# Kernel tuning notes

Hardware: AMD Instinct MI355X
Metric: run time of the kernel (lower is better)

Reference implementation:

```python
import jax, jax.numpy as jnp
import numpy as np

B, L, D = 16, 1024, 1024
OUT_LEN = 24
N_LAYERS = 3
CYCLE = L
LN_EPS = 1e-5


def _make_pe(seq_len, hidden, cycle):
    # pe[t, j] = 2*pi*t/cycle, then sin on even cols, cos on odd cols
    t = jnp.arange(seq_len, dtype=jnp.float32)[:, None]
    base = (2.0 * jnp.pi * t / cycle) * jnp.ones((1, hidden), jnp.float32)
    cols = jnp.arange(hidden)
    return jnp.where((cols % 2 == 0)[None, :], jnp.sin(base), jnp.cos(base))


def setup_inputs() -> dict:
    key = jax.random.key(0)
    ks = jax.random.split(key, 12)
    s = 0.02
    return {
        "x": jax.random.normal(ks[0], (B, L, D), jnp.float32),
        "pe": _make_pe(L, D, CYCLE),
        "w1": jax.random.normal(ks[1], (N_LAYERS, D, D), jnp.float32) * s,
        "b1": jnp.zeros((N_LAYERS, D), jnp.float32),
        "w2": jax.random.normal(ks[2], (N_LAYERS, D, D), jnp.float32) * s,
        "b2": jnp.zeros((N_LAYERS, D), jnp.float32),
        "ln_g": jnp.ones((N_LAYERS, D), jnp.float32),
        "ln_b": jnp.zeros((N_LAYERS, D), jnp.float32),
        "fc_w": jax.random.normal(ks[3], (1, D), jnp.float32) * s,
        "fc_b": jnp.zeros((1,), jnp.float32),
        "final_w": jax.random.normal(ks[4], (OUT_LEN, L), jnp.float32) * s,
        "final_b": jnp.zeros((OUT_LEN,), jnp.float32),
    }


def _layer_norm(y, g, b):
    mu = jnp.mean(y, axis=-1, keepdims=True)
    var = jnp.mean((y - mu) ** 2, axis=-1, keepdims=True)
    return (y - mu) * jax.lax.rsqrt(var + LN_EPS) * g + b


def reference(x, pe, w1, b1, w2, b2, ln_g, ln_b, fc_w, fc_b, final_w, final_b):
    d = x.shape[-1]
    scale = 1.0 / jnp.sqrt(jnp.float32(d))
    # positional add (pe[:, :seq_len]; here L == D so this is the full buffer)
    h = x + pe[:, : x.shape[1]]
    attns = []
    for l in range(w1.shape[0]):
        # hand-rolled bmm-softmax-bmm self-attention (q = k = v = h)
        scores = jnp.einsum("bqd,bkd->bqk", h, h) * scale  # (B, L, L)
        a = jax.nn.softmax(scores, axis=-1)
        ctx = jnp.einsum("bqk,bkd->bqd", a, h)
        # position-wise FFN with hidden == D, residual over ctx, then LN
        ff = jnp.maximum(ctx @ w1[l].T + b1[l], 0.0) @ w2[l].T + b2[l]
        h = _layer_norm(ctx + ff, ln_g[l], ln_b[l])
        attns.append(a)
    # final head: D -> 1, squeeze, then L -> OUT_LEN over the sequence dim
    z = (h @ fc_w.T + fc_b)[..., 0]  # (B, L)
    out = z @ final_w.T + final_b    # (B, OUT_LEN)
    return (out, jnp.stack(attns))
```

## Files before the change

### kernel.cpp

```cpp
#include <hip/hip_runtime.h>

typedef unsigned short u16;
typedef __attribute__((ext_vector_type(8))) short short8;
typedef __attribute__((ext_vector_type(4))) float f32x4;
typedef __attribute__((ext_vector_type(4))) unsigned short u16x4;

__device__ __forceinline__ float bf2f(u16 u){
  union { unsigned int i; float f; } x; x.i = ((unsigned int)u) << 16; return x.f;
}
__device__ __forceinline__ u16 f2bf(float f){
  union { float f; unsigned int i; } x; x.f = f;
  return (u16)((x.i + 0x7fffu + ((x.i >> 16) & 1u)) >> 16);
}
__device__ __forceinline__ void async16(const void* g, void* s){
  __builtin_amdgcn_global_load_lds((const __attribute__((address_space(1))) void*)g,
                                   (__attribute__((address_space(3))) void*)s, 16, 0, 0);
}

__global__ __launch_bounds__(256) void k_split2(const float* __restrict__ s1, u16* __restrict__ d1,
                                                const float* __restrict__ s2, u16* __restrict__ d2){
  long i = ((long)blockIdx.x * 256 + threadIdx.x) * 4;
  f32x4 v1 = *(const f32x4*)(s1 + i);
  f32x4 v2 = *(const f32x4*)(s2 + i);
  u16x4 h1, h2;
  #pragma unroll
  for (int j=0;j<4;j++){ h1[j] = f2bf(v1[j]); h2[j] = f2bf(v2[j]); }
  *(u16x4*)(d1+i) = h1;
  *(u16x4*)(d2+i) = h2;
}

__global__ __launch_bounds__(256) void k_addpe(const float* __restrict__ x, const float* __restrict__ pe,
                                               u16* __restrict__ d){
  long i = ((long)blockIdx.x * 256 + threadIdx.x) * 4;
  f32x4 xv = *(const f32x4*)(x + i);
  f32x4 pv = *(const f32x4*)(pe + (i & 1048575));
  u16x4 hh;
  #pragma unroll
  for (int j=0;j<4;j++) hh[j] = f2bf(xv[j]+pv[j]);
  *(u16x4*)(d+i) = hh;
}

__global__ __launch_bounds__(256) void k_transpose(const u16* __restrict__ in, u16* __restrict__ outp){
  __shared__ u16 tile[64][68];
  const long b = blockIdx.z;
  const int d0 = blockIdx.x * 64, l0 = blockIdx.y * 64;
  const long ibase = b * 1048576l;
  const int t = threadIdx.x;
  const int cr = t >> 4;
  const int cc = (t & 15) * 4;
  #pragma unroll
  for (int rr=0; rr<4; rr++){
    int row = cr + rr*16;
    u16x4 v = *(const u16x4*)(in + ibase + (long)(l0+row)*1024 + d0 + cc);
    *(u16x4*)&tile[row][cc] = v;
  }
  __syncthreads();
  #pragma unroll
  for (int rr=0; rr<4; rr++){
    int drow = cr + rr*16;
    u16x4 y;
    y[0] = tile[cc+0][drow];
    y[1] = tile[cc+1][drow];
    y[2] = tile[cc+2][drow];
    y[3] = tile[cc+3][drow];
    *(u16x4*)(outp + ibase + (long)(d0+drow)*1024 + l0 + cc) = y;
  }
}

__global__ __launch_bounds__(512, 1) void attn_sm(
    const u16* __restrict__ hB, float* __restrict__ probs, u16* __restrict__ pB)
{
  __shared__ __align__(16) u16 sm[65536];
  const int t = threadIdx.x;
  const int w = t >> 6, lane = t & 63;
  const int fr = lane & 15, fs = lane >> 4;

  const int p = blockIdx.x;
  const int id = (p & 7) * 32 + (p >> 3);
  const long bz = id >> 4;
  const int brow = (id & 15) << 6;

  const u16* hb = hB + bz * 1048576l;

  const u16* gsrc[8];
  int gdst[8];
  #pragma unroll
  for (int c=0;c<8;c++){
    int u = c*512 + t;
    int row = u >> 2;
    int slot = (u & 3) ^ ((row >> 1) & 3);
    gsrc[c] = hb + (long)row*1024 + slot*8;
    gdst[c] = c*4096 + w*512;
  }

  int offA[4], offB[8];
  #pragma unroll
  for (int i=0;i<4;i++){
    int x = i*16 + fr;
    offA[i] = (brow + x)*32 + (fs ^ (((brow + x)>>1)&3))*8;
  }
  #pragma unroll
  for (int j=0;j<8;j++){
    int x = w*128 + j*16 + fr;
    offB[j] = x*32 + (fs ^ ((x>>1)&3))*8;
  }

  f32x4 acc[4][8];
  #pragma unroll
  for (int i=0;i<4;i++)
    #pragma unroll
    for (int j=0;j<8;j++) acc[i][j] = (f32x4){0.f,0.f,0.f,0.f};

  #pragma unroll
  for (int c=0;c<8;c++) async16(gsrc[c], sm + gdst[c]);
  asm volatile("s_waitcnt vmcnt(0)" ::: "memory");
  __builtin_amdgcn_s_barrier();
  __builtin_amdgcn_sched_barrier(0);

#define ATT_BODY(BUF)                                                          \
    short8 aF[4], bF[8];                                                       \
    _Pragma("unroll")                                                          \
    for (int i=0;i<4;i++) aF[i] = *(const short8*)((BUF) + offA[i]);           \
    _Pragma("unroll")                                                          \
    for (int j=0;j<8;j++) bF[j] = *(const short8*)((BUF) + offB[j]);           \
    __builtin_amdgcn_s_setprio(1);                                             \
    _Pragma("unroll")                                                          \
    for (int i=0;i<4;i++)                                                      \
      _Pragma("unroll")                                                        \
      for (int j=0;j<8;j++)                                                    \
        acc[i][j] = __builtin_amdgcn_mfma_f32_16x16x32_bf16(aF[i], bF[j], acc[i][j], 0,0,0); \
    __builtin_amdgcn_s_setprio(0);

  for (int kt = 0; kt < 31; ++kt){
    const u16* buf = sm + (kt & 1)*32768;
    u16* stg = sm + ((kt + 1) & 1)*32768;
    const int ko = (kt + 1)*32;
    #pragma unroll
    for (int c=0;c<8;c++) async16(gsrc[c] + ko, stg + gdst[c]);
    ATT_BODY(buf)
    asm volatile("s_waitcnt vmcnt(0)" ::: "memory");
    __builtin_amdgcn_s_barrier();
    __builtin_amdgcn_sched_barrier(0);
  }
  {
    const u16* buf = sm + 32768;
    ATT_BODY(buf)
  }
#undef ATT_BODY

  float* red = (float*)sm;
  const float SC = 0.03125f;

  float mx[4][4];
  #pragma unroll
  for (int i=0;i<4;i++)
    #pragma unroll
    for (int q=0;q<4;q++){
      float m = acc[i][0][q];
      #pragma unroll
      for (int j=1;j<8;j++) m = fmaxf(m, acc[i][j][q]);
      #pragma unroll
      for (int d=1; d<16; d<<=1) m = fmaxf(m, __shfl_xor(m, d));
      mx[i][q] = m;
    }
  if (fr == 0){
    #pragma unroll
    for (int i=0;i<4;i++)
      #pragma unroll
      for (int q=0;q<4;q++) red[(i*16 + fs*4 + q)*8 + w] = mx[i][q];
  }
  __syncthreads();
  float M[4][4];
  #pragma unroll
  for (int i=0;i<4;i++)
    #pragma unroll
    for (int q=0;q<4;q++){
      const int row = i*16 + fs*4 + q;
      f32x4 a = *(const f32x4*)&red[row*8];
      f32x4 b = *(const f32x4*)&red[row*8+4];
      M[i][q] = fmaxf(fmaxf(fmaxf(a[0],a[1]),fmaxf(a[2],a[3])),
                      fmaxf(fmaxf(b[0],b[1]),fmaxf(b[2],b[3])));
    }
  float sum[4][4];
  #pragma unroll
  for (int i=0;i<4;i++)
    #pragma unroll
    for (int q=0;q<4;q++){
      float s = 0.f;
      #pragma unroll
      for (int j=0;j<8;j++){
        float e = expf((acc[i][j][q] - M[i][q]) * SC);
        acc[i][j][q] = e;
        s += e;
      }
      #pragma unroll
      for (int d=1; d<16; d<<=1) s += __shfl_xor(s, d);
      sum[i][q] = s;
    }
  __syncthreads();
  if (fr == 0){
    #pragma unroll
    for (int i=0;i<4;i++)
      #pragma unroll
      for (int q=0;q<4;q++) red[(i*16 + fs*4 + q)*8 + w] = sum[i][q];
  }
  __syncthreads();
  float inv[4][4];
  #pragma unroll
  for (int i=0;i<4;i++)
    #pragma unroll
    for (int q=0;q<4;q++){
      const int row = i*16 + fs*4 + q;
      f32x4 a = *(const f32x4*)&red[row*8];
      f32x4 b = *(const f32x4*)&red[row*8+4];
      inv[i][q] = 1.0f / (a[0]+a[1]+a[2]+a[3]+b[0]+b[1]+b[2]+b[3]);
    }

  const long obase = bz * 1048576l;
  #pragma unroll
  for (int i=0;i<4;i++)
    #pragma unroll
    for (int q=0;q<4;q++){
      const long rbase = obase + (long)(brow + i*16 + fs*4 + q)*1024;
      const float iv = inv[i][q];
      #pragma unroll
      for (int j=0;j<8;j++){
        const int col = w*128 + j*16 + fr;
        const float pv = acc[i][j][q] * iv;
        probs[rbase + col] = pv;
        pB[rbase + col] = f2bf(pv);
      }
    }
}

template<int MODE>
__global__ __launch_bounds__(512, 2) void gemm8(
    const u16* __restrict__ aB, const u16* __restrict__ bB,
    int per, long sA, long sB, long sC,
    int lda, int ldb, int ldc,
    float scale, const float* __restrict__ bias,
    const u16* __restrict__ res,
    float* __restrict__ cF, u16* __restrict__ cB)
{
  __shared__ __align__(16) u16 sm[65536];
  const int t = threadIdx.x;
  const int w = t >> 6, lane = t & 63;
  const int wm = w >> 2, wn = w & 3;
  const int fr = lane & 15, fs = lane >> 4;

  const int p = blockIdx.x;
  const int chunk = gridDim.x >> 3;
  const int id = (p & 7) * chunk + (p >> 3);
  const long bz = id / per;
  const int rem = id % per;
  const int m0 = (rem >> 2) << 8, n0 = (rem & 3) << 8;

  const u16* a = aB + bz * sA;
  const u16* b = bB + bz * sB;

  const int urow = t >> 2;
  const int col8 = ((t & 3) ^ ((t >> 3) & 3)) * 8;
  const u16* gA0 = a + (long)(m0 + urow) * lda + col8;
  const u16* gA1 = a + (long)(m0 + 128 + urow) * lda + col8;
  const u16* gB0 = b + (long)(n0 + urow) * ldb + col8;
  const u16* gB1 = b + (long)(n0 + 128 + urow) * ldb + col8;
  u16* dA0 = sm + (w << 9);
  u16* dA1 = sm + 4096 + (w << 9);
  u16* dB0 = sm + 8192 + (w << 9);
  u16* dB1 = sm + 12288 + (w << 9);

  int offA[8], offB[4];
  #pragma unroll
  for (int i=0;i<8;i++){
    int row = wm*128 + i*16 + fr;
    int sl = fs ^ ((row >> 1) & 3);
    offA[i] = row*32 + sl*8;
  }
  #pragma unroll
  for (int j=0;j<4;j++){
    int row = wn*64 + j*16 + fr;
    int sl = fs ^ ((row >> 1) & 3);
    offB[j] = 8192 + row*32 + sl*8;
  }

  f32x4 acc[8][4];
  #pragma unroll
  for (int i=0;i<8;i++)
    #pragma unroll
    for (int j=0;j<4;j++) acc[i][j] = (f32x4){0.f,0.f,0.f,0.f};

  #pragma unroll
  for (int pb=0; pb<3; ++pb){
    const int kb = pb*32, sb = pb*16384;
    async16(gA0+kb, dA0+sb); async16(gA1+kb, dA1+sb);
    async16(gB0+kb, dB0+sb); async16(gB1+kb, dB1+sb);
  }
  gA0 += 96; gA1 += 96; gB0 += 96; gB1 += 96;
  asm volatile("s_waitcnt vmcnt(8)" ::: "memory");
  __builtin_amdgcn_s_barrier();
  __builtin_amdgcn_sched_barrier(0);

#define KT_PHASE(SMB, I0, I1, STG, RDB)                                        \
  { short8 a0 = *(const short8*)((SMB) + offA[I0]);                            \
    short8 a1 = *(const short8*)((SMB) + offA[I1]);                            \
    RDB                                                                        \
    STG                                                                        \
    __builtin_amdgcn_sched_barrier(0);                                         \
    __builtin_amdgcn_s_barrier();                                              \
    __builtin_amdgcn_sched_barrier(0);                                         \
    __builtin_amdgcn_s_setprio(1);                                             \
    acc[I0][0] = __builtin_amdgcn_mfma_f32_16x16x32_bf16(a0, bF[0], acc[I0][0], 0,0,0); \
    acc[I0][1] = __builtin_amdgcn_mfma_f32_16x16x32_bf16(a0, bF[1], acc[I0][1], 0,0,0); \
    acc[I0][2] = __builtin_amdgcn_mfma_f32_16x16x32_bf16(a0, bF[2], acc[I0][2], 0,0,0); \
    acc[I0][3] = __builtin_amdgcn_mfma_f32_16x16x32_bf16(a0, bF[3], acc[I0][3], 0,0,0); \
    acc[I1][0] = __builtin_amdgcn_mfma_f32_16x16x32_bf16(a1, bF[0], acc[I1][0], 0,0,0); \
    acc[I1][1] = __builtin_amdgcn_mfma_f32_16x16x32_bf16(a1, bF[1], acc[I1][1], 0,0,0); \
    acc[I1][2] = __builtin_amdgcn_mfma_f32_16x16x32_bf16(a1, bF[2], acc[I1][2], 0,0,0); \
    acc[I1][3] = __builtin_amdgcn_mfma_f32_16x16x32_bf16(a1, bF[3], acc[I1][3], 0,0,0); \
    __builtin_amdgcn_s_setprio(0);                                             \
  }

#define KT_BODY4(SMB, ST0, ST1, ST2, ST3)                                      \
  { short8 bF[4];                                                              \
    KT_PHASE(SMB, 0, 1, ST0,                                                   \
      { bF[0] = *(const short8*)((SMB) + offB[0]);                             \
        bF[1] = *(const short8*)((SMB) + offB[1]);                             \
        bF[2] = *(const short8*)((SMB) + offB[2]);                             \
        bF[3] = *(const short8*)((SMB) + offB[3]); })                          \
    KT_PHASE(SMB, 2, 3, ST1, {})                                               \
    KT_PHASE(SMB, 4, 5, ST2, {})                                               \
    KT_PHASE(SMB, 6, 7, ST3, {})                                               \
  }

  for (int kt = 0; kt < 29; ++kt){
    const u16* smb = sm + (kt & 3)*16384;
    const int sb = ((kt + 3) & 3)*16384;
    KT_BODY4(smb,
      { async16(gA0, dA0+sb); gA0 += 32; },
      { async16(gA1, dA1+sb); gA1 += 32; },
      { async16(gB0, dB0+sb); gB0 += 32; },
      { async16(gB1, dB1+sb); gB1 += 32; })
    asm volatile("s_waitcnt vmcnt(8)" ::: "memory");
    __builtin_amdgcn_s_barrier();
    __builtin_amdgcn_sched_barrier(0);
  }
  {
    const u16* smb = sm + (29 & 3)*16384;
    KT_BODY4(smb, {}, {}, {}, {})
    asm volatile("s_waitcnt vmcnt(4)" ::: "memory");
    __builtin_amdgcn_s_barrier();
    __builtin_amdgcn_sched_barrier(0);
  }
  {
    const u16* smb = sm + (30 & 3)*16384;
    KT_BODY4(smb, {}, {}, {}, {})
    asm volatile("s_waitcnt vmcnt(0)" ::: "memory");
    __builtin_amdgcn_s_barrier();
    __builtin_amdgcn_sched_barrier(0);
  }
  {
    const u16* smb = sm + (31 & 3)*16384;
    KT_BODY4(smb, {}, {}, {}, {})
  }
#undef KT_BODY4
#undef KT_PHASE

  const long cBase = bz * sC;
  const int rb = m0 + wm*128 + fs*4;
  const int cb = n0 + wn*64 + fr;
  #pragma unroll
  for (int j=0;j<4;j++){
    const int c = cb + j*16;
    float bv = 0.f;
    if constexpr (MODE == 2 || MODE == 3) bv = bias[c];
    #pragma unroll
    for (int i=0;i<8;i++){
      #pragma unroll
      for (int q=0;q<4;q++){
        const int r = rb + i*16 + q;
        const long idx = cBase + (long)r*ldc + c;
        float v = acc[i][j][q];
        if constexpr (MODE == 1){
          cB[idx] = f2bf(v);
        } else if constexpr (MODE == 2){
          cB[idx] = f2bf(fmaxf(v + bv, 0.f));
        } else {
          cF[idx] = v + bv + bf2f(res[idx]);
        }
      }
    }
  }
}

__global__ __launch_bounds__(256) void k_ln(const float* __restrict__ r,
                                            const float* __restrict__ g, const float* __restrict__ b,
                                            u16* __restrict__ h){
  const long row = blockIdx.x;
  const float* rr = r + row * 1024;
  const int t = threadIdx.x, w = t >> 6, lane = t & 63;
  __shared__ float rA[4], rB[4];
  f32x4 v = *(const f32x4*)(rr + t*4);
  float s = v[0]+v[1]+v[2]+v[3];
  #pragma unroll
  for (int off=32; off; off>>=1) s += __shfl_xor(s, off);
  if (lane==0) rA[w] = s;
  __syncthreads();
  const float mu = (rA[0]+rA[1]+rA[2]+rA[3]) * (1.0f/1024.0f);
  float sq = 0.f;
  #pragma unroll
  for (int j=0;j<4;j++){ float d = v[j]-mu; sq += d*d; }
  #pragma unroll
  for (int off=32; off; off>>=1) sq += __shfl_xor(sq, off);
  if (lane==0) rB[w] = sq;
  __syncthreads();
  const float var = (rB[0]+rB[1]+rB[2]+rB[3]) * (1.0f/1024.0f);
  const float inv = rsqrtf(var + 1e-5f);
  u16x4 hh;
  #pragma unroll
  for (int j=0;j<4;j++){
    int d = t*4+j;
    hh[j] = f2bf((v[j]-mu)*inv*g[d] + b[d]);
  }
  *(u16x4*)(h + row*1024 + t*4) = hh;
}

__global__ __launch_bounds__(256) void k_final1(const u16* __restrict__ h,
                                                const float* __restrict__ fw, const float* __restrict__ fb,
                                                float* __restrict__ z){
  const int row = blockIdx.x*4 + (threadIdx.x>>6);
  const int lane = threadIdx.x & 63;
  const long base = (long)row * 1024;
  const int d0 = lane * 16;
  float s = 0.f;
  #pragma unroll
  for (int j=0;j<16;j++){
    int d = d0 + j;
    s += bf2f(h[base+d]) * fw[d];
  }
  #pragma unroll
  for (int off=32; off; off>>=1) s += __shfl_xor(s, off);
  if (lane==0) z[row] = s + fb[0];
}

__global__ __launch_bounds__(256) void k_final2(const float* __restrict__ z,
                                                const float* __restrict__ fw, const float* __restrict__ fb,
                                                float* __restrict__ out){
  const int idx = blockIdx.x*4 + (threadIdx.x>>6);
  const int lane = threadIdx.x & 63;
  const int b = idx / 24, o = idx % 24;
  float s = 0.f;
  #pragma unroll
  for (int j=0;j<16;j++){
    int li = lane + j*64;
    s += z[b*1024 + li] * fw[o*1024 + li];
  }
  #pragma unroll
  for (int off=32; off; off>>=1) s += __shfl_xor(s, off);
  if (lane==0) out[idx] = s + fb[o];
}

extern "C" void kernel_launch(void* const* d_in, const int* in_sizes, int n_in,
                              void* d_out, int out_size, void* d_ws, size_t ws_size,
                              hipStream_t stream){
  const float* x   = (const float*)d_in[0];
  const float* pe  = (const float*)d_in[1];
  const float* w1  = (const float*)d_in[2];
  const float* b1  = (const float*)d_in[3];
  const float* w2  = (const float*)d_in[4];
  const float* b2  = (const float*)d_in[5];
  const float* lng = (const float*)d_in[6];
  const float* lnb = (const float*)d_in[7];
  const float* fcw = (const float*)d_in[8];
  const float* fcb = (const float*)d_in[9];
  const float* fw  = (const float*)d_in[10];
  const float* fb  = (const float*)d_in[11];
  float* out  = (float*)d_out;
  float* attn = out + 384;

  char* ws = (char*)d_ws;
  const long BB = 32l*1024*1024;
  u16* hB = (u16*)(ws + 0*BB);
  u16* tB = (u16*)(ws + 1*BB);
  u16* cB = (u16*)(ws + 2*BB);
  u16* pB = (u16*)(ws + 3*BB);
  float* rf = (float*)(ws + 4*BB);
  u16* w1B = (u16*)(ws + 6*BB);
  u16* w2B = w1B + 3l*1024*1024;
  float* z = (float*)(w2B + 3l*1024*1024);

  const long M1 = 1024l*1024;

  k_split2<<<3072, 256, 0, stream>>>(w1, w1B, w2, w2B);
  k_addpe<<<16384, 256, 0, stream>>>(x, pe, hB);
  k_transpose<<<dim3(16,16,16), 256, 0, stream>>>(hB, tB);

  for (int l = 0; l < 3; l++){
    float* sc = attn + (long)l*16*M1;
    attn_sm<<<256, 512, 0, stream>>>(hB, sc, pB);
    gemm8<1><<<256, 512, 0, stream>>>(pB, tB, 16, M1,M1,M1, 1024,1024,1024,
        1.f, nullptr, nullptr, nullptr, cB);
    gemm8<2><<<256, 512, 0, stream>>>(cB, w1B+l*M1, 256, 0,0,0, 1024,1024,1024,
        1.f, b1+l*1024, nullptr, nullptr, pB);
    gemm8<3><<<256, 512, 0, stream>>>(pB, w2B+l*M1, 256, 0,0,0, 1024,1024,1024,
        1.f, b2+l*1024, cB, rf, nullptr);
    k_ln<<<16384, 256, 0, stream>>>(rf, lng+l*1024, lnb+l*1024, hB);
    if (l < 2) k_transpose<<<dim3(16,16,16), 256, 0, stream>>>(hB, tB);
  }

  k_final1<<<4096, 256, 0, stream>>>(hB, fcw, fcb, z);
  k_final2<<<96, 256, 0, stream>>>(z, fw, fb, out);
}
```

Measured before the change: 726.3 us.

## Fuse pos-add with transpose and LayerNorm with transpose, store residual as bf16

Result: slower. 831.0 us (+14.4%).

```diff
diff --git a/kernel.cpp b/kernel.cpp
--- a/kernel.cpp
+++ b/kernel.cpp
@@ -29,18 +29,8 @@
   *(u16x4*)(d2+i) = h2;
 }
 
-__global__ __launch_bounds__(256) void k_addpe(const float* __restrict__ x, const float* __restrict__ pe,
-                                               u16* __restrict__ d){
-  long i = ((long)blockIdx.x * 256 + threadIdx.x) * 4;
-  f32x4 xv = *(const f32x4*)(x + i);
-  f32x4 pv = *(const f32x4*)(pe + (i & 1048575));
-  u16x4 hh;
-  #pragma unroll
-  for (int j=0;j<4;j++) hh[j] = f2bf(xv[j]+pv[j]);
-  *(u16x4*)(d+i) = hh;
-}
-
-__global__ __launch_bounds__(256) void k_transpose(const u16* __restrict__ in, u16* __restrict__ outp){
+__global__ __launch_bounds__(256) void k_addpet(const float* __restrict__ x, const float* __restrict__ pe,
+                                                u16* __restrict__ hB, u16* __restrict__ tB){
   __shared__ u16 tile[64][68];
   const long b = blockIdx.z;
   const int d0 = blockIdx.x * 64, l0 = blockIdx.y * 64;
@@ -51,8 +41,14 @@
   #pragma unroll
   for (int rr=0; rr<4; rr++){
     int row = cr + rr*16;
-    u16x4 v = *(const u16x4*)(in + ibase + (long)(l0+row)*1024 + d0 + cc);
-    *(u16x4*)&tile[row][cc] = v;
+    long off = (long)(l0+row)*1024 + d0 + cc;
+    f32x4 xv = *(const f32x4*)(x + ibase + off);
+    f32x4 pv = *(const f32x4*)(pe + off);
+    u16x4 hh;
+    #pragma unroll
+    for (int j=0;j<4;j++) hh[j] = f2bf(xv[j]+pv[j]);
+    *(u16x4*)(hB + ibase + off) = hh;
+    *(u16x4*)&tile[row][cc] = hh;
   }
   __syncthreads();
   #pragma unroll
@@ -63,7 +59,7 @@
     y[1] = tile[cc+1][drow];
     y[2] = tile[cc+2][drow];
     y[3] = tile[cc+3][drow];
-    *(u16x4*)(outp + ibase + (long)(d0+drow)*1024 + l0 + cc) = y;
+    *(u16x4*)(tB + ibase + (long)(d0+drow)*1024 + l0 + cc) = y;
   }
 }
 
@@ -237,10 +233,8 @@
 __global__ __launch_bounds__(512, 2) void gemm8(
     const u16* __restrict__ aB, const u16* __restrict__ bB,
     int per, long sA, long sB, long sC,
-    int lda, int ldb, int ldc,
-    float scale, const float* __restrict__ bias,
-    const u16* __restrict__ res,
-    float* __restrict__ cF, u16* __restrict__ cB)
+    const float* __restrict__ bias, const u16* __restrict__ res,
+    u16* __restrict__ cB)
 {
   __shared__ __align__(16) u16 sm[65536];
   const int t = threadIdx.x;
@@ -260,10 +254,10 @@
 
   const int urow = t >> 2;
   const int col8 = ((t & 3) ^ ((t >> 3) & 3)) * 8;
-  const u16* gA0 = a + (long)(m0 + urow) * lda + col8;
-  const u16* gA1 = a + (long)(m0 + 128 + urow) * lda + col8;
-  const u16* gB0 = b + (long)(n0 + urow) * ldb + col8;
-  const u16* gB1 = b + (long)(n0 + 128 + urow) * ldb + col8;
+  const u16* gA0 = a + (long)(m0 + urow) * 1024 + col8;
+  const u16* gA1 = a + (long)(m0 + 128 + urow) * 1024 + col8;
+  const u16* gB0 = b + (long)(n0 + urow) * 1024 + col8;
+  const u16* gB1 = b + (long)(n0 + 128 + urow) * 1024 + col8;
   u16* dA0 = sm + (w << 9);
   u16* dA1 = sm + 4096 + (w << 9);
   u16* dB0 = sm + 8192 + (w << 9);
@@ -378,50 +372,86 @@
       #pragma unroll
       for (int q=0;q<4;q++){
         const int r = rb + i*16 + q;
-        const long idx = cBase + (long)r*ldc + c;
+        const long idx = cBase + (long)r*1024 + c;
         float v = acc[i][j][q];
         if constexpr (MODE == 1){
           cB[idx] = f2bf(v);
         } else if constexpr (MODE == 2){
           cB[idx] = f2bf(fmaxf(v + bv, 0.f));
         } else {
-          cF[idx] = v + bv + bf2f(res[idx]);
+          cB[idx] = f2bf(v + bv + bf2f(res[idx]));
         }
       }
     }
   }
 }
 
-__global__ __launch_bounds__(256) void k_ln(const float* __restrict__ r,
-                                            const float* __restrict__ g, const float* __restrict__ b,
-                                            u16* __restrict__ h){
-  const long row = blockIdx.x;
-  const float* rr = r + row * 1024;
-  const int t = threadIdx.x, w = t >> 6, lane = t & 63;
-  __shared__ float rA[4], rB[4];
-  f32x4 v = *(const f32x4*)(rr + t*4);
-  float s = v[0]+v[1]+v[2]+v[3];
-  #pragma unroll
-  for (int off=32; off; off>>=1) s += __shfl_xor(s, off);
-  if (lane==0) rA[w] = s;
+__global__ __launch_bounds__(256) void k_lnt(const u16* __restrict__ r,
+                                             const float* __restrict__ g, const float* __restrict__ b,
+                                             u16* __restrict__ h, u16* __restrict__ tp){
+  __shared__ u16 tile[64][68];
+  __shared__ float smu[64], sinv[64];
+  const long bz = blockIdx.y;
+  const int l0 = blockIdx.x * 64;
+  const long ibase = bz * 1048576l;
+  const int t = threadIdx.x;
+  const int w = t >> 6, lane = t & 63;
+
+  for (int rr = 0; rr < 16; ++rr){
+    const int row = w*16 + rr;
+    const u16* rp = r + ibase + (long)(l0+row)*1024 + lane*16;
+    short8 v0 = *(const short8*)(rp);
+    short8 v1 = *(const short8*)(rp + 8);
+    float s = 0.f, sq = 0.f;
+    #pragma unroll
+    for (int j=0;j<8;j++){
+      float a = bf2f((u16)v0[j]), c = bf2f((u16)v1[j]);
+      s += a + c; sq += a*a + c*c;
+    }
+    #pragma unroll
+    for (int off=32; off; off>>=1){ s += __shfl_xor(s, off); sq += __shfl_xor(sq, off); }
+    if (lane == 0){
+      const float mu = s * (1.0f/1024.0f);
+      const float var = sq * (1.0f/1024.0f) - mu*mu;
+      smu[row] = mu;
+      sinv[row] = rsqrtf(var + 1e-5f);
+    }
+  }
   __syncthreads();
-  const float mu = (rA[0]+rA[1]+rA[2]+rA[3]) * (1.0f/1024.0f);
-  float sq = 0.f;
-  #pragma unroll
-  for (int j=0;j<4;j++){ float d = v[j]-mu; sq += d*d; }
-  #pragma unroll
-  for (int off=32; off; off>>=1) sq += __shfl_xor(sq, off);
-  if (lane==0) rB[w] = sq;
-  __syncthreads();
-  const float var = (rB[0]+rB[1]+rB[2]+rB[3]) * (1.0f/1024.0f);
-  const float inv = rsqrtf(var + 1e-5f);
-  u16x4 hh;
-  #pragma unroll
-  for (int j=0;j<4;j++){
-    int d = t*4+j;
-    hh[j] = f2bf((v[j]-mu)*inv*g[d] + b[d]);
-  }
-  *(u16x4*)(h + row*1024 + t*4) = hh;
+
+  const int cr = t >> 4;
+  const int cc = (t & 15) * 4;
+  for (int c = 0; c < 16; ++c){
+    const int d0 = c * 64;
+    f32x4 gv = *(const f32x4*)(g + d0 + cc);
+    f32x4 bv = *(const f32x4*)(b + d0 + cc);
+    #pragma unroll
+    for (int rr=0; rr<4; rr++){
+      int row = cr + rr*16;
+      const float mu = smu[row], inv = sinv[row];
+      long off = ibase + (long)(l0+row)*1024 + d0 + cc;
+      u16x4 rv = *(const u16x4*)(r + off);
+      u16x4 hh;
+      #pragma unroll
+      for (int j=0;j<4;j++) hh[j] = f2bf((bf2f(rv[j])-mu)*inv*gv[j] + bv[j]);
+      *(u16x4*)(h + off) = hh;
+      if (tp) *(u16x4*)&tile[row][cc] = hh;
+    }
+    if (tp){
+      __syncthreads();
+      #pragma unroll
+      for (int rr=0; rr<4; rr++){
+        int drow = cr + rr*16;
+        u16x4 y;
+        y[0] = tile[cc+0][drow];
+        y[1] = tile[cc+1][drow];
+        y[2] = tile[cc+2][drow];
+        y[3] = tile[cc+3][drow];
+        *(u16x4*)(tp + ibase + (long)(d0+drow)*1024 + l0 + cc) = y;
+      }
+      __syncthreads();
+    }
+  }
 }
 
 __global__ __launch_bounds__(256) void k_final1(const u16* __restrict__ h,
@@ -483,7 +513,7 @@
   u16* tB = (u16*)(ws + 1*BB);
   u16* cB = (u16*)(ws + 2*BB);
   u16* pB = (u16*)(ws + 3*BB);
-  float* rf = (float*)(ws + 4*BB);
+  u16* rfB = (u16*)(ws + 4*BB);
   u16* w1B = (u16*)(ws + 6*BB);
   u16* w2B = w1B + 3l*1024*1024;
   float* z = (float*)(w2B + 3l*1024*1024);
@@ -491,20 +521,19 @@
   const long M1 = 1024l*1024;
 
   k_split2<<<3072, 256, 0, stream>>>(w1, w1B, w2, w2B);
-  k_addpe<<<16384, 256, 0, stream>>>(x, pe, hB);
-  k_transpose<<<dim3(16,16,16), 256, 0, stream>>>(hB, tB);
+  k_addpet<<<dim3(16,16,16), 256, 0, stream>>>(x, pe, hB, tB);
 
   for (int l = 0; l < 3; l++){
     float* sc = attn + (long)l*16*M1;
     attn_sm<<<256, 512, 0, stream>>>(hB, sc, pB);
-    gemm8<1><<<256, 512, 0, stream>>>(pB, tB, 16, M1,M1,M1, 1024,1024,1024,
-        1.f, nullptr, nullptr, nullptr, cB);
-    gemm8<2><<<256, 512, 0, stream>>>(cB, w1B+l*M1, 256, 0,0,0, 1024,1024,1024,
-        1.f, b1+l*1024, nullptr, nullptr, pB);
-    gemm8<3><<<256, 512, 0, stream>>>(pB, w2B+l*M1, 256, 0,0,0, 1024,1024,1024,
-        1.f, b2+l*1024, cB, rf, nullptr);
-    k_ln<<<16384, 256, 0, stream>>>(rf, lng+l*1024, lnb+l*1024, hB);
-    if (l < 2) k_transpose<<<dim3(16,16,16), 256, 0, stream>>>(hB, tB);
+    gemm8<1><<<256, 512, 0, stream>>>(pB, tB, 16, M1,M1,M1,
+        nullptr, nullptr, cB);
+    gemm8<2><<<256, 512, 0, stream>>>(cB, w1B+l*M1, 256, 0,0,0,
+        b1+l*1024, nullptr, pB);
+    gemm8<3><<<256, 512, 0, stream>>>(pB, w2B+l*M1, 256, 0,0,0,
+        b2+l*1024, cB, rfB);
+    k_lnt<<<dim3(16,16), 256, 0, stream>>>(rfB, lng+l*1024, lnb+l*1024, hB,
+        (l < 2) ? tB : (u16*)nullptr);
   }
 
   k_final1<<<4096, 256, 0, stream>>>(hB, fcw, fcb, z);
```
